# Kernel tuning notes

Measured on AMD Instinct MI355X. Metric: run time of the kernel, lower is better.

The kernel has to match this reference:

```python
import jax, jax.numpy as jnp
import numpy as np

N_HEAD = 16
WINDOW = 16  # fixed_window_size


def setup_inputs() -> dict:
    key = jax.random.key(0)
    k1, k2, k3 = jax.random.split(key, 3)
    B, T, C = 2, 2048, 1024
    x = jax.random.normal(k1, (B, T, C), dtype=jnp.float32)
    # torch Linear(C, 3C, bias=False): y = x @ W.T with W [3C, C].
    # We store the pre-transposed [C, 3C] matrix so y = x @ w_qkv.
    w_qkv = jax.random.normal(k2, (C, 3 * C), dtype=jnp.float32) * (1.0 / np.sqrt(C))
    w_proj = jax.random.normal(k3, (C, C), dtype=jnp.float32) * (1.0 / np.sqrt(C))
    return {"x": x, "w_qkv": w_qkv, "w_proj": w_proj}


def reference(x, w_qkv, w_proj):
    B, T, C = x.shape
    H, D = N_HEAD, C // N_HEAD
    qkv = x @ w_qkv  # [B, T, 3C]
    q, k, v = jnp.split(qkv, 3, axis=-1)
    # [B, T, C] -> [B, H, T, D]
    q, k, v = (t.reshape(B, T, H, D).transpose(0, 2, 1, 3) for t in (q, k, v))
    att = jnp.einsum("bhtd,bhsd->bhts", q, k) * (1.0 / np.sqrt(D))  # [B,H,T,T]
    # Mask exactly as the torch module builds it: tril ones, then zero where
    # col - row >= fixed_window_size (note: col-row, per the source).
    row = jnp.arange(T)[:, None]
    col = jnp.arange(T)[None, :]
    mask = (col <= row) & ~(col - row >= WINDOW)  # [T, T] bool
    att = jnp.where(mask[None, None, :, :], att, -jnp.inf)
    att = jax.nn.softmax(att, axis=-1)
    y = jnp.einsum("bhts,bhsd->bhtd", att, v)  # [B,H,T,D]
    y = y.transpose(0, 2, 1, 3).reshape(B, T, C)
    return y @ w_proj
```

## Files before the change

kernel.cpp:

```cpp
#include <hip/hip_runtime.h>
#include <stdint.h>

#define LOG2E 1.4426950408889634f
#define QSCALE 0.18033688011112042f

typedef __attribute__((ext_vector_type(8))) short bf16x8;
typedef __attribute__((ext_vector_type(4))) float f32x4;
typedef __attribute__((ext_vector_type(8))) unsigned short u16x8;

#define B_ 2
#define T_ 2048
#define C_ 1024
#define H_ 16
#define D_ 64
#define BT_ 4096
#define N3_ 3072

#if __has_builtin(__builtin_amdgcn_exp2f)
#define EXP2(x) __builtin_amdgcn_exp2f(x)
#else
#define EXP2(x) exp2f(x)
#endif

__device__ __forceinline__ unsigned short f2bf(float f) {
  union { float f; unsigned u; } x; x.f = f;
  return (unsigned short)((x.u + 0x7fffu + ((x.u >> 16) & 1u)) >> 16);
}
__device__ __forceinline__ float bf2f(unsigned short u) {
  union { unsigned u; float f; } x; x.u = ((unsigned)u) << 16;
  return x.f;
}
__device__ __forceinline__ unsigned f2u(float f) {
  union { float f; unsigned u; } x; x.f = f; return x.u;
}
__device__ __forceinline__ unsigned pack_bf2(float a, float b) {
  return __builtin_amdgcn_perm(f2u(b) + 0x8000u, f2u(a) + 0x8000u, 0x07060302u);
}

__device__ __forceinline__ void gld16(const unsigned short* g, unsigned short* l) {
  __builtin_amdgcn_global_load_lds(
      (const __attribute__((address_space(1))) unsigned int*)g,
      (__attribute__((address_space(3))) unsigned int*)l, 16, 0, 0);
}

__global__ void cvt_kernel(const float* __restrict__ in, unsigned short* __restrict__ out, int n) {
  int i = (blockIdx.x * blockDim.x + threadIdx.x) * 4;
  if (i >= n) return;
  float4 v = *(const float4*)(in + i);
  ushort4 o;
  o.x = f2bf(v.x); o.y = f2bf(v.y); o.z = f2bf(v.z); o.w = f2bf(v.w);
  *(ushort4*)(out + i) = o;
}

__global__ void tr_kernel(const float* __restrict__ in, unsigned short* __restrict__ out, int K, int N) {
  __shared__ unsigned short tile[32][33];
  int n0 = blockIdx.x * 32, k0 = blockIdx.y * 32;
  int tx = threadIdx.x, ty = threadIdx.y;
  tile[ty][tx] = f2bf(in[(size_t)(k0 + ty) * N + n0 + tx]);
  __syncthreads();
  out[(size_t)(n0 + ty) * K + k0 + tx] = tile[tx][ty];
}

template <int MODE>
__global__ __launch_bounds__(256) void gemm_kernel(
    const unsigned short* __restrict__ A, const unsigned short* __restrict__ Bt,
    unsigned short* __restrict__ qo, unsigned short* __restrict__ ko,
    unsigned short* __restrict__ vo, float* __restrict__ fo) {
  __shared__ unsigned short As[128 * 64];
  __shared__ unsigned short Bs[64 * 64];
  const int tid = threadIdx.x;
  const int wave = tid >> 6, lane = tid & 63;
  const int quad = lane >> 4, l16 = lane & 15;
  const int wm = (wave >> 1) * 64, wn = (wave & 1) * 32;
  const int m0 = blockIdx.y * 128, n0 = blockIdx.x * 64;

  f32x4 acc[4][2] = {};

  for (int k = 0; k < 1024; k += 64) {
    __syncthreads();
#pragma unroll
    for (int i = 0; i < 4; i++) {
      const int s = tid + 256 * i;
      const int row = s >> 3, ch = s & 7;
      gld16(A + (size_t)(m0 + row) * 1024 + k + ((ch ^ (row & 7)) * 8), As + s * 8);
    }
#pragma unroll
    for (int i = 0; i < 2; i++) {
      const int s = tid + 256 * i;
      const int row = s >> 3, ch = s & 7;
      gld16(Bt + (size_t)(n0 + row) * 1024 + k + ((ch ^ (row & 7)) * 8), Bs + s * 8);
    }
    __syncthreads();
#pragma unroll
    for (int sub = 0; sub < 2; sub++) {
      bf16x8 af[4], bfr[2];
#pragma unroll
      for (int mi = 0; mi < 4; mi++) {
        const int row = wm + mi * 16 + l16;
        af[mi] = *(const bf16x8*)(As + row * 64 + (((sub * 4 + quad) ^ (row & 7)) * 8));
      }
#pragma unroll
      for (int ni = 0; ni < 2; ni++) {
        const int row = wn + ni * 16 + l16;
        bfr[ni] = *(const bf16x8*)(Bs + row * 64 + (((sub * 4 + quad) ^ (row & 7)) * 8));
      }
#pragma unroll
      for (int mi = 0; mi < 4; mi++)
#pragma unroll
        for (int ni = 0; ni < 2; ni++)
          acc[mi][ni] = __builtin_amdgcn_mfma_f32_16x16x32_bf16(af[mi], bfr[ni], acc[mi][ni], 0, 0, 0);
    }
  }

  if (MODE == 0) {
    const int part = n0 >> 10;
    const int hh = (n0 >> 6) & 15;
#pragma unroll
    for (int mi = 0; mi < 4; mi++) {
#pragma unroll
      for (int r = 0; r < 4; r++) {
        const int m = m0 + wm + mi * 16 + quad * 4 + r;
        const int b = m >> 11, t = m & 2047;
#pragma unroll
        for (int ni = 0; ni < 2; ni++) {
          const int d = wn + ni * 16 + l16;
          float val = acc[mi][ni][r];
          if (part == 0) val *= QSCALE;
          const unsigned short bv = f2bf(val);
          if (part == 0)
            qo[((size_t)(b * H_ + hh) * T_ + t) * D_ + d] = bv;
          else if (part == 1)
            ko[((size_t)(b * H_ + hh) * T_ + t) * D_ + d] = bv;
          else
            vo[((size_t)(b * H_ + hh) * D_ + d) * T_ + t] = bv;
        }
      }
    }
  } else {
#pragma unroll
    for (int mi = 0; mi < 4; mi++)
#pragma unroll
      for (int r = 0; r < 4; r++) {
        const int m = m0 + wm + mi * 16 + quad * 4 + r;
#pragma unroll
        for (int ni = 0; ni < 2; ni++)
          fo[(size_t)m * 1024 + n0 + wn + ni * 16 + l16] = acc[mi][ni][r];
      }
  }
}

__global__ __launch_bounds__(256) void attn_kernel(
    const unsigned short* __restrict__ qb, const unsigned short* __restrict__ kb,
    const unsigned short* __restrict__ vb, unsigned short* __restrict__ yb,
    unsigned short* __restrict__ po, float* __restrict__ pl) {
  const int tid = threadIdx.x;
  const int wave = tid >> 6, lane = tid & 63;
  const int quad = lane >> 4, l16 = lane & 15;

  const int bid = blockIdx.x;
  const int bh = bid & 31;
  const int u = 62 - (bid >> 5);
  int qs, c, nch;
  if (u < 11) { qs = u; c = 0; nch = 1; }
  else if (u < 33) { int v = u - 11; qs = 11 + (v >> 1); c = v & 1; nch = 2; }
  else { int v = u - 33; qs = 22 + v / 3; c = v % 3; nch = 3; }
  const int nt = qs + 1;
  const int j0 = c * nt / nch, j1 = (c + 1) * nt / nch;
  const int b = bh >> 4, h = bh & 15;

  __shared__ unsigned short Ks[64 * 64];
  __shared__ unsigned short Vt[64 * 64];
  __shared__ unsigned short Ps[4 * 16 * 68];
  unsigned short* Pw = Ps + wave * 16 * 68;

  const unsigned short* Qg = qb + (size_t)bh * T_ * D_;
  const unsigned short* Kg = kb + (size_t)bh * T_ * D_;
  const unsigned short* Vg = vb + (size_t)bh * D_ * T_;

  const unsigned short* qp = Qg + (size_t)(qs * 64 + wave * 16 + l16) * D_ + quad * 8;
  bf16x8 qf0 = *(const bf16x8*)qp, qf1 = *(const bf16x8*)(qp + 32);

  f32x4 o[4] = {};
  float lacc = 0.f;
  const int qglob = qs * 64 + wave * 16 + l16;
  const int sloc_base = quad * 4;

  const int trow = tid >> 3, tch = tid & 7;

  for (int jt = j0; jt < j1; jt++) {
    const int s0 = jt * 64;
    __syncthreads();
    {
      const int r0 = trow, r1 = trow + 32;
      gld16(Kg + (size_t)(s0 + r0) * D_ + ((tch ^ (r0 & 7)) * 8), Ks + r0 * 64 + tch * 8);
      gld16(Kg + (size_t)(s0 + r1) * D_ + ((tch ^ (r1 & 7)) * 8), Ks + r1 * 64 + tch * 8);
      gld16(Vg + (size_t)r0 * T_ + s0 + ((tch ^ (r0 & 7)) * 8), Vt + r0 * 64 + tch * 8);
      gld16(Vg + (size_t)r1 * T_ + s0 + ((tch ^ (r1 & 7)) * 8), Vt + r1 * 64 + tch * 8);
    }
    __syncthreads();

    f32x4 s[4];
#pragma unroll
    for (int mi = 0; mi < 4; mi++) {
      const int row = mi * 16 + l16, sw = row & 7;
      bf16x8 kf0 = *(const bf16x8*)(Ks + row * 64 + ((quad ^ sw) * 8));
      bf16x8 kf1 = *(const bf16x8*)(Ks + row * 64 + (((quad + 4) ^ sw) * 8));
      f32x4 z = {0.f, 0.f, 0.f, 0.f};
      z = __builtin_amdgcn_mfma_f32_16x16x32_bf16(kf0, qf0, z, 0, 0, 0);
      s[mi] = __builtin_amdgcn_mfma_f32_16x16x32_bf16(kf1, qf1, z, 0, 0, 0);
    }

    if (jt == qs) {
#pragma unroll
      for (int mi = 0; mi < 4; mi++)
#pragma unroll
        for (int r = 0; r < 4; r++) {
          float p = EXP2(s[mi][r]);
          p = (s0 + mi * 16 + sloc_base + r > qglob) ? 0.f : p;
          s[mi][r] = p;
          lacc += p;
        }
    } else {
#pragma unroll
      for (int mi = 0; mi < 4; mi++)
#pragma unroll
        for (int r = 0; r < 4; r++) {
          float p = EXP2(s[mi][r]);
          s[mi][r] = p;
          lacc += p;
        }
    }

#pragma unroll
    for (int mi = 0; mi < 4; mi++) {
      unsigned d0 = pack_bf2(s[mi][0], s[mi][1]);
      unsigned d1 = pack_bf2(s[mi][2], s[mi][3]);
      *(uint2*)(Pw + l16 * 68 + mi * 16 + quad * 4) = make_uint2(d0, d1);
    }

#pragma unroll
    for (int kk = 0; kk < 2; kk++) {
      bf16x8 pf = *(const bf16x8*)(Pw + l16 * 68 + kk * 32 + quad * 8);
#pragma unroll
      for (int ni = 0; ni < 4; ni++) {
        const int row = ni * 16 + l16, sw = row & 7;
        bf16x8 vf = *(const bf16x8*)(Vt + row * 64 + (((kk * 4 + quad) ^ sw) * 8));
        o[ni] = __builtin_amdgcn_mfma_f32_16x16x32_bf16(pf, vf, o[ni], 0, 0, 0);
      }
    }
  }

  lacc += __shfl_xor(lacc, 16, 64);
  lacc += __shfl_xor(lacc, 32, 64);
  float lr[4];
#pragma unroll
  for (int r = 0; r < 4; r++) lr[r] = __shfl(lacc, quad * 4 + r, 16);

  if (nch == 1) {
#pragma unroll
    for (int r = 0; r < 4; r++) {
      float inv = 1.0f / lr[r];
      int tq = qs * 64 + wave * 16 + quad * 4 + r;
#pragma unroll
      for (int ni = 0; ni < 4; ni++)
        yb[((size_t)(b * T_ + tq)) * 1024 + h * 64 + ni * 16 + l16] = f2bf(o[ni][r] * inv);
    }
  } else {
    const int slot = 52 * bh + ((qs <= 21) ? ((qs - 11) * 2 + c) : (22 + (qs - 22) * 3 + c));
    unsigned short* pob = po + (size_t)slot * 4096;
#pragma unroll
    for (int r = 0; r < 4; r++) {
      const int row64 = wave * 16 + quad * 4 + r;
#pragma unroll
      for (int ni = 0; ni < 4; ni++)
        pob[row64 * 64 + ni * 16 + l16] = f2bf(o[ni][r]);
      if (l16 == 0) pl[slot * 64 + row64] = lr[r];
    }
  }
}

__global__ __launch_bounds__(256) void reduce_kernel(
    const unsigned short* __restrict__ po, const float* __restrict__ pl,
    unsigned short* __restrict__ yb) {
  int idx = blockIdx.x * 256 + threadIdx.x;
  int bh = idx / 21504;
  int rem = idx - bh * 21504;
  int rr = rem >> 4, cg = rem & 15;
  int qs = 11 + (rr >> 6), row64 = rr & 63;
  int base, nch;
  if (qs <= 21) { base = (qs - 11) * 2; nch = 2; }
  else { base = 22 + (qs - 22) * 3; nch = 3; }
  int b = bh >> 4, h = bh & 15;
  float a0 = 0.f, a1 = 0.f, a2 = 0.f, a3 = 0.f, l = 0.f;
  for (int cc = 0; cc < nch; cc++) {
    int slot = 52 * bh + base + cc;
    const unsigned short* p = po + (size_t)slot * 4096 + row64 * 64 + cg * 4;
    ushort4 uv = *(const ushort4*)p;
    a0 += bf2f(uv.x); a1 += bf2f(uv.y); a2 += bf2f(uv.z); a3 += bf2f(uv.w);
    l += pl[slot * 64 + row64];
  }
  float inv = 1.0f / l;
  int tq = qs * 64 + row64;
  ushort4 w;
  w.x = f2bf(a0 * inv); w.y = f2bf(a1 * inv); w.z = f2bf(a2 * inv); w.w = f2bf(a3 * inv);
  *(ushort4*)(yb + ((size_t)(b * T_ + tq)) * 1024 + h * 64 + cg * 4) = w;
}

extern "C" void kernel_launch(void* const* d_in, const int* in_sizes, int n_in,
                              void* d_out, int out_size, void* d_ws, size_t ws_size,
                              hipStream_t stream) {
  const float* x = (const float*)d_in[0];
  const float* w_qkv = (const float*)d_in[1];
  const float* w_proj = (const float*)d_in[2];
  float* out = (float*)d_out;

  unsigned short* xb = (unsigned short*)d_ws;
  unsigned short* wprojT = xb + (size_t)BT_ * C_;
  unsigned short* qb = wprojT + (size_t)C_ * C_;
  unsigned short* kb = qb + (size_t)B_ * H_ * T_ * D_;
  unsigned short* vb = kb + (size_t)B_ * H_ * T_ * D_;
  unsigned short* wqkvT = vb + (size_t)B_ * H_ * T_ * D_;
  unsigned short* po = wqkvT;
  float* pl = (float*)(po + (size_t)1664 * 4096);
  unsigned short* yb = xb;

  cvt_kernel<<<(BT_ * C_ / 4 + 255) / 256, 256, 0, stream>>>(x, xb, BT_ * C_);
  dim3 trb(32, 32);
  tr_kernel<<<dim3(N3_ / 32, C_ / 32), trb, 0, stream>>>(w_qkv, wqkvT, C_, N3_);
  tr_kernel<<<dim3(C_ / 32, C_ / 32), trb, 0, stream>>>(w_proj, wprojT, C_, C_);

  gemm_kernel<0><<<dim3(N3_ / 64, BT_ / 128), 256, 0, stream>>>(xb, wqkvT, qb, kb, vb, nullptr);
  attn_kernel<<<dim3(32 * 63), 256, 0, stream>>>(qb, kb, vb, yb, po, pl);
  reduce_kernel<<<dim3(2688), 256, 0, stream>>>(po, pl, yb);
  gemm_kernel<1><<<dim3(C_ / 64, BT_ / 128), 256, 0, stream>>>(yb, wprojT, nullptr, nullptr, nullptr, out);
}
```

Before: 199.4 us.

## Fuse prep kernels into one launch and load GEMM B operand directly to registers

Merges the x conversion and both weight transposes into a single prep kernel with 256-thread blocks, each thread handling four rows of the transpose. This cuts two kernel launches and uses smaller blocks. In the GEMM, the B tile no longer goes through shared memory: each lane loads its MFMA B fragments straight from global memory into registers, which removes the LDS traffic and shared-memory footprint for B. The cost is uncoalesced, redundant global reads of B across the waves that share it, and those loads may not overlap as well as the async LDS path did.

```diff
diff --git a/kernel.cpp b/kernel.cpp
--- a/kernel.cpp
+++ b/kernel.cpp
@@ -43,22 +43,38 @@
       (__attribute__((address_space(3))) unsigned int*)l, 16, 0, 0);
 }
 
-__global__ void cvt_kernel(const float* __restrict__ in, unsigned short* __restrict__ out, int n) {
-  int i = (blockIdx.x * blockDim.x + threadIdx.x) * 4;
-  if (i >= n) return;
-  float4 v = *(const float4*)(in + i);
-  ushort4 o;
-  o.x = f2bf(v.x); o.y = f2bf(v.y); o.z = f2bf(v.z); o.w = f2bf(v.w);
-  *(ushort4*)(out + i) = o;
-}
-
-__global__ void tr_kernel(const float* __restrict__ in, unsigned short* __restrict__ out, int K, int N) {
+__device__ __forceinline__ void tr32(const float* __restrict__ in,
+                                     unsigned short* __restrict__ out,
+                                     int K, int N, int b, int nbx, int tid) {
   __shared__ unsigned short tile[32][33];
-  int n0 = blockIdx.x * 32, k0 = blockIdx.y * 32;
-  int tx = threadIdx.x, ty = threadIdx.y;
-  tile[ty][tx] = f2bf(in[(size_t)(k0 + ty) * N + n0 + tx]);
+  const int bx = b % nbx, by = b / nbx;
+  const int n0 = bx * 32, k0 = by * 32;
+  const int tx = tid & 31, ty = (tid >> 5) * 4;
+#pragma unroll
+  for (int r = 0; r < 4; r++)
+    tile[ty + r][tx] = f2bf(in[(size_t)(k0 + ty + r) * N + n0 + tx]);
   __syncthreads();
-  out[(size_t)(n0 + ty) * K + k0 + tx] = tile[tx][ty];
+#pragma unroll
+  for (int r = 0; r < 4; r++)
+    out[(size_t)(n0 + ty + r) * K + k0 + tx] = tile[tx][ty + r];
+}
+
+__global__ __launch_bounds__(256) void prep_kernel(
+    const float* __restrict__ x, unsigned short* __restrict__ xb,
+    const float* __restrict__ wq, unsigned short* __restrict__ wqT,
+    const float* __restrict__ wp, unsigned short* __restrict__ wpT) {
+  const int bid = blockIdx.x, tid = threadIdx.x;
+  if (bid < 4096) {
+    int i = (bid * 256 + tid) * 4;
+    float4 v = *(const float4*)(x + i);
+    ushort4 o;
+    o.x = f2bf(v.x); o.y = f2bf(v.y); o.z = f2bf(v.z); o.w = f2bf(v.w);
+    *(ushort4*)(xb + i) = o;
+  } else if (bid < 4096 + 3072) {
+    tr32(wq, wqT, 1024, 3072, bid - 4096, 96, tid);
+  } else {
+    tr32(wp, wpT, 1024, 1024, bid - 7168, 32, tid);
+  }
 }
 
 template <int MODE>
@@ -67,7 +83,6 @@
     unsigned short* __restrict__ qo, unsigned short* __restrict__ ko,
     unsigned short* __restrict__ vo, float* __restrict__ fo) {
   __shared__ unsigned short As[128 * 64];
-  __shared__ unsigned short Bs[64 * 64];
   const int tid = threadIdx.x;
   const int wave = tid >> 6, lane = tid & 63;
   const int quad = lane >> 4, l16 = lane & 15;
@@ -76,6 +91,9 @@
 
   f32x4 acc[4][2] = {};
 
+  const unsigned short* Bp0 = Bt + (size_t)(n0 + wn + l16) * 1024 + quad * 8;
+  const unsigned short* Bp1 = Bp0 + 16 * 1024;
+
   for (int k = 0; k < 1024; k += 64) {
     __syncthreads();
 #pragma unroll
@@ -84,31 +102,26 @@
       const int row = s >> 3, ch = s & 7;
       gld16(A + (size_t)(m0 + row) * 1024 + k + ((ch ^ (row & 7)) * 8), As + s * 8);
     }
-#pragma unroll
-    for (int i = 0; i < 2; i++) {
-      const int s = tid + 256 * i;
-      const int row = s >> 3, ch = s & 7;
-      gld16(Bt + (size_t)(n0 + row) * 1024 + k + ((ch ^ (row & 7)) * 8), Bs + s * 8);
-    }
+    bf16x8 b00 = *(const bf16x8*)(Bp0 + k);
+    bf16x8 b01 = *(const bf16x8*)(Bp1 + k);
+    bf16x8 b10 = *(const bf16x8*)(Bp0 + k + 32);
+    bf16x8 b11 = *(const bf16x8*)(Bp1 + k + 32);
     __syncthreads();
 #pragma unroll
     for (int sub = 0; sub < 2; sub++) {
-      bf16x8 af[4], bfr[2];
+      bf16x8 af[4];
 #pragma unroll
       for (int mi = 0; mi < 4; mi++) {
         const int row = wm + mi * 16 + l16;
         af[mi] = *(const bf16x8*)(As + row * 64 + (((sub * 4 + quad) ^ (row & 7)) * 8));
       }
-#pragma unroll
-      for (int ni = 0; ni < 2; ni++) {
-        const int row = wn + ni * 16 + l16;
-        bfr[ni] = *(const bf16x8*)(Bs + row * 64 + (((sub * 4 + quad) ^ (row & 7)) * 8));
-      }
-#pragma unroll
-      for (int mi = 0; mi < 4; mi++)
-#pragma unroll
-        for (int ni = 0; ni < 2; ni++)
-          acc[mi][ni] = __builtin_amdgcn_mfma_f32_16x16x32_bf16(af[mi], bfr[ni], acc[mi][ni], 0, 0, 0);
+      const bf16x8 bz0 = sub ? b10 : b00;
+      const bf16x8 bz1 = sub ? b11 : b01;
+#pragma unroll
+      for (int mi = 0; mi < 4; mi++) {
+        acc[mi][0] = __builtin_amdgcn_mfma_f32_16x16x32_bf16(af[mi], bz0, acc[mi][0], 0, 0, 0);
+        acc[mi][1] = __builtin_amdgcn_mfma_f32_16x16x32_bf16(af[mi], bz1, acc[mi][1], 0, 0, 0);
+      }
     }
   }
 
@@ -324,10 +337,7 @@
   float* pl = (float*)(po + (size_t)1664 * 4096);
   unsigned short* yb = xb;
 
-  cvt_kernel<<<(BT_ * C_ / 4 + 255) / 256, 256, 0, stream>>>(x, xb, BT_ * C_);
-  dim3 trb(32, 32);
-  tr_kernel<<<dim3(N3_ / 32, C_ / 32), trb, 0, stream>>>(w_qkv, wqkvT, C_, N3_);
-  tr_kernel<<<dim3(C_ / 32, C_ / 32), trb, 0, stream>>>(w_proj, wprojT, C_, C_);
+  prep_kernel<<<dim3(8192), 256, 0, stream>>>(x, xb, w_qkv, wqkvT, w_proj, wprojT);
 
   gemm_kernel<0><<<dim3(N3_ / 64, BT_ / 128), 256, 0, stream>>>(xb, wqkvT, qb, kb, vb, nullptr);
   attn_kernel<<<dim3(32 * 63), 256, 0, stream>>>(qb, kb, vb, yb, po, pl);
```

Measured after the change: 218.9 us. +9.8%, slower.
